# Kernel tuning notes

Measured on AMD Instinct MI355X. Metric: run time of the kernel, lower is better.

Reference implementation:

```python
import jax, jax.numpy as jnp
import numpy as np

MAX_ITER = 10
F_TOL = 1e-8
FREE_NUM = 100  # free_idx[1] + 1
OUT_DIM = 512


def setup_inputs() -> dict:
    key = jax.random.key(0)
    ks = jax.random.split(key, 13)
    f32 = jnp.float32
    b = jax.random.normal(ks[0], (64, 448), f32)
    # MLP params (nn.Linear convention: W [out, in], bias [out])
    W1 = jax.random.normal(ks[1], (1024, 448), f32) * 0.05
    b1 = jax.random.normal(ks[2], (1024,), f32) * 0.01
    W2 = jax.random.normal(ks[3], (1024, 1024), f32) * 0.03
    b2 = jax.random.normal(ks[4], (1024,), f32) * 0.01
    W3 = jax.random.normal(ks[5], (1024, 1024), f32) * 0.03
    b3 = jax.random.normal(ks[6], (1024,), f32) * 0.01
    W4 = jax.random.normal(ks[7], (512, 1024), f32) * 0.03
    b4 = jax.random.normal(ks[8], (512,), f32) * 0.01
    A = jax.random.normal(ks[9], (448, 512), f32) * 0.05
    WzProj = jax.random.normal(ks[10], (512, 512), f32) * 0.01  # contractive
    WbProj = jax.random.normal(ks[11], (512, 448), f32) * 0.05
    return {"b": b, "W1": W1, "b1": b1, "W2": W2, "b2": b2, "W3": W3,
            "b3": b3, "W4": W4, "b4": b4, "A": A, "WzProj": WzProj,
            "WbProj": WbProj}


def _projection(out, b0, A, WzProj, WbProj):
    # Fixed-point projection with on-device convergence flag + Jacobian accum
    bsz = out.shape[0]
    Bias = b0 @ WbProj.T                     # [bsz, d]
    col = jnp.arange(OUT_DIM)
    J0 = jnp.broadcast_to(jnp.eye(OUT_DIM, dtype=out.dtype),
                          (bsz, OUT_DIM, OUT_DIM))
    def cond(st):
        _, _, it, done = st
        return (it <= MAX_ITER) & (~done)
    def body(st):
        z, J, it, _ = st
        z = Bias + z @ WzProj.T
        # rows to clamp: negative AND in the ReLU (non-free) block
        mask = (z < 0) & (col >= FREE_NUM)                 # [bsz, d]
        J_iter = jnp.where(mask[:, :, None], 0.0, WzProj[None])  # [bsz,d,d]
        J = jnp.einsum('bij,bjk->bik', J_iter, J)          # bmm
        z = jnp.where(mask, 0.0, z)                        # u, relu(v)
        worst = jnp.max(jnp.abs(z @ A.T - b0))             # inf-norm residual
        return (z, J, it + 1, worst <= F_TOL)
    z, J, _, _ = jax.lax.while_loop(
        cond, body, (out, J0, jnp.int32(1), jnp.array(False)))
    return z, J


def reference(b, W1, b1, W2, b2, W3, b3, W4, b4, A, WzProj, WbProj):
    b0 = b
    h = b  # truncate_idx = [0, 448] -> full slice
    h = jax.nn.relu(h @ W1.T + b1)
    h = jax.nn.relu(h @ W2.T + b2)
    h = jax.nn.relu(h @ W3.T + b3)
    out = h @ W4.T + b4                                    # [bsz, 512]
    z_star, _ = _projection(out, b0, A, WzProj, WbProj)
    return (z_star, out)
```

## Files before the change

kernel.cpp:

```cpp
#include <hip/hip_runtime.h>


#define FREE0 100

__global__ __launch_bounds__(256) void transpose512(
    const float* __restrict__ Wz, float* __restrict__ WzT)
{
    __shared__ __align__(16) float Ts[64][65];
    const int t  = threadIdx.x;
    const int k0 = (blockIdx.x >> 3) * 64;
    const int n0 = (blockIdx.x & 7) * 64;
    #pragma unroll
    for (int i = 0; i < 4; ++i) {
        int f  = i * 256 + t;
        int r  = f >> 4;
        int c4 = (f & 15) << 2;
        const float4 v =
            *reinterpret_cast<const float4*>(Wz + (n0 + r) * 512 + k0 + c4);
        Ts[c4 + 0][r] = v.x; Ts[c4 + 1][r] = v.y;
        Ts[c4 + 2][r] = v.z; Ts[c4 + 3][r] = v.w;
    }
    __syncthreads();
    #pragma unroll
    for (int i = 0; i < 4; ++i) {
        int f   = i * 256 + t;
        int kk  = f >> 4;
        int nn4 = (f & 15) << 2;
        float4 w;
        w.x = Ts[kk][nn4 + 0]; w.y = Ts[kk][nn4 + 1];
        w.z = Ts[kk][nn4 + 2]; w.w = Ts[kk][nn4 + 3];
        *reinterpret_cast<float4*>(WzT + (k0 + kk) * 512 + n0 + nn4) = w;
    }
}

template <bool PRE>
__global__ __launch_bounds__(256) void linearSK(
    const float* __restrict__ X,
    const float* __restrict__ bp,
    const float* __restrict__ W,
    float* __restrict__ Cp,
    int N, int K, int chunk)
{
    __shared__ float Xs[64][65];
    __shared__ __align__(16) float Ws[64][16];

    const int t   = threadIdx.x;
    const int m   = t & 63;
    const int wv  = t >> 6;
    const int n0  = blockIdx.x * 16;
    const int kb  = blockIdx.y * chunk;
    const int ke  = (kb + chunk < K) ? (kb + chunk) : K;

    const int xc4 = (t & 15) << 2;
    const int xr0 = t >> 4;
    const int wnr = t >> 4;
    const int wkc = (t & 15) << 2;

    float4 xr[4];
    float4 wr;
    float4 bpv = {0.f, 0.f, 0.f, 0.f};

    auto issue = [&](int k0) {
        #pragma unroll
        for (int s = 0; s < 4; ++s)
            xr[s] = *reinterpret_cast<const float4*>(
                X + (s * 16 + xr0) * K + k0 + xc4);
        wr = *reinterpret_cast<const float4*>(W + (n0 + wnr) * K + k0 + wkc);
        if (PRE)
            bpv = *reinterpret_cast<const float4*>(bp + k0 + xc4);
    };

    issue(kb);
    float4 acc = {0.f, 0.f, 0.f, 0.f};

    for (int k0 = kb; k0 < ke; k0 += 64) {
        #pragma unroll
        for (int s = 0; s < 4; ++s) {
            float4 v = xr[s];
            if (PRE) {
                v.x = fmaxf(v.x + bpv.x, 0.f);
                v.y = fmaxf(v.y + bpv.y, 0.f);
                v.z = fmaxf(v.z + bpv.z, 0.f);
                v.w = fmaxf(v.w + bpv.w, 0.f);
            }
            const int row = s * 16 + xr0;
            Xs[xc4 + 0][row] = v.x; Xs[xc4 + 1][row] = v.y;
            Xs[xc4 + 2][row] = v.z; Xs[xc4 + 3][row] = v.w;
        }
        Ws[wkc + 0][wnr] = wr.x; Ws[wkc + 1][wnr] = wr.y;
        Ws[wkc + 2][wnr] = wr.z; Ws[wkc + 3][wnr] = wr.w;
        __syncthreads();

        if (k0 + 64 < ke) issue(k0 + 64);

        #pragma unroll 16
        for (int kk = 0; kk < 64; ++kk) {
            const float  xa = Xs[kk][m];
            const float4 w4 =
                *reinterpret_cast<const float4*>(&Ws[kk][wv * 4]);
            acc.x = fmaf(xa, w4.x, acc.x);
            acc.y = fmaf(xa, w4.y, acc.y);
            acc.z = fmaf(xa, w4.z, acc.z);
            acc.w = fmaf(xa, w4.w, acc.w);
        }
        __syncthreads();
    }

    float* cb = Cp + m * N + n0 + wv * 4;
    atomicAdd(cb + 0, acc.x);
    atomicAdd(cb + 1, acc.y);
    atomicAdd(cb + 2, acc.z);
    atomicAdd(cb + 3, acc.w);
}

__global__ __launch_bounds__(1024) void zloop2(
    const float* __restrict__ pre4,
    const float* __restrict__ b4,
    const float* __restrict__ WzT,
    const float* __restrict__ bz,
    float* __restrict__ dout)
{
    __shared__ float part[16][2][512];
    __shared__ float zs[512][2];
    __shared__ float bs[2][512];

    const int t   = threadIdx.x;
    const int bid = blockIdx.x;
    const int r   = t >> 9;
    const int c   = t & 511;
    const int row = bid * 2 + r;

    {
        const float z0 = pre4[row * 512 + c] + b4[c];
        dout[32768 + row * 512 + c] = z0;
        zs[c][r] = z0;
        bs[r][c] = bz[row * 512 + c];
    }
    __syncthreads();

    const int wv = t >> 6;
    const int l  = t & 63;
    const float* wbase = WzT + (wv * 32) * 512 + l * 8;

    for (int it = 0; it < 10; ++it) {
        float4 a00 = {0,0,0,0}, a01 = {0,0,0,0};
        float4 a10 = {0,0,0,0}, a11 = {0,0,0,0};
        const float* wp = wbase;
        #pragma unroll 4
        for (int kk = 0; kk < 32; ++kk) {
            const float4 w0 = *reinterpret_cast<const float4*>(wp);
            const float4 w1 = *reinterpret_cast<const float4*>(wp + 4);
            const float2 zr =
                *reinterpret_cast<const float2*>(&zs[wv * 32 + kk][0]);
            a00.x = fmaf(zr.x, w0.x, a00.x);
            a00.y = fmaf(zr.x, w0.y, a00.y);
            a00.z = fmaf(zr.x, w0.z, a00.z);
            a00.w = fmaf(zr.x, w0.w, a00.w);
            a01.x = fmaf(zr.x, w1.x, a01.x);
            a01.y = fmaf(zr.x, w1.y, a01.y);
            a01.z = fmaf(zr.x, w1.z, a01.z);
            a01.w = fmaf(zr.x, w1.w, a01.w);
            a10.x = fmaf(zr.y, w0.x, a10.x);
            a10.y = fmaf(zr.y, w0.y, a10.y);
            a10.z = fmaf(zr.y, w0.z, a10.z);
            a10.w = fmaf(zr.y, w0.w, a10.w);
            a11.x = fmaf(zr.y, w1.x, a11.x);
            a11.y = fmaf(zr.y, w1.y, a11.y);
            a11.z = fmaf(zr.y, w1.z, a11.z);
            a11.w = fmaf(zr.y, w1.w, a11.w);
            wp += 512;
        }
        *reinterpret_cast<float4*>(&part[wv][0][l * 8    ]) = a00;
        *reinterpret_cast<float4*>(&part[wv][0][l * 8 + 4]) = a01;
        *reinterpret_cast<float4*>(&part[wv][1][l * 8    ]) = a10;
        *reinterpret_cast<float4*>(&part[wv][1][l * 8 + 4]) = a11;
        __syncthreads();

        float v = bs[r][c];
        #pragma unroll
        for (int w = 0; w < 16; ++w) v += part[w][r][c];
        if (c >= FREE0) v = fmaxf(v, 0.f);
        zs[c][r] = v;
        if (it == 9) dout[row * 512 + c] = v;
        __syncthreads();
    }
}

extern "C" void kernel_launch(void* const* d_in, const int* in_sizes, int n_in,
                              void* d_out_v, int out_size, void* d_ws,
                              size_t ws_size, hipStream_t stream)
{
    const float* b  = (const float*)d_in[0];
    const float* W1 = (const float*)d_in[1];
    const float* b1 = (const float*)d_in[2];
    const float* W2 = (const float*)d_in[3];
    const float* b2 = (const float*)d_in[4];
    const float* W3 = (const float*)d_in[5];
    const float* b3 = (const float*)d_in[6];
    const float* W4 = (const float*)d_in[7];
    const float* b4 = (const float*)d_in[8];
    const float* Wz = (const float*)d_in[10];
    const float* Wb = (const float*)d_in[11];

    float* out = (float*)d_out_v;
    float* f   = (float*)d_ws;
    float* WzT  = f;
    float* z0b  = f + 262144;
    float* h1   = z0b;
    float* h2   = h1 + 65536;
    float* h3   = h2 + 65536;
    float* outp = h3 + 65536;
    float* bzv  = outp + 32768;

    hipMemsetAsync(z0b, 0, 262144 * sizeof(float), stream);
    transpose512<<<64, 256, 0, stream>>>(Wz, WzT);

    linearSK<false><<<dim3(64, 2), 256, 0, stream>>>(b,  nullptr, W1, h1,
                                                     1024, 448, 256);
    linearSK<true ><<<dim3(64, 4), 256, 0, stream>>>(h1, b1, W2, h2,
                                                     1024, 1024, 256);
    linearSK<true ><<<dim3(64, 4), 256, 0, stream>>>(h2, b2, W3, h3,
                                                     1024, 1024, 256);
    linearSK<true ><<<dim3(32, 4), 256, 0, stream>>>(h3, b3, W4, outp,
                                                     512, 1024, 256);
    linearSK<false><<<dim3(32, 2), 256, 0, stream>>>(b,  nullptr, Wb, bzv,
                                                     512, 448, 256);

    zloop2<<<32, 1024, 0, stream>>>(outp, b4, WzT, bzv, out);
}
```

Measured before the change: 247.1 us.

## Replace split-K atomic GEMMs with in-block K reduction and fused stage kernel

Replaces the split-K linear kernels, which relied on a memset and atomicAdd, with 1024-thread blocks that each compute 4 output columns across the full K. Partial sums are reduced in shared memory and the bias and ReLU are applied in the epilogue. The Wz transpose, the Wb projection and the first layer are merged into one stage0 launch, and the fixed-point loop now prefetches weights into registers. This removes the memset, the atomics and several launches, but the small-column-per-block layout reads W with strided scalar loads and reuses data less.

Result: slower. 477.7 us (+93.4%).

```diff
diff --git a/kernel.cpp b/kernel.cpp
--- a/kernel.cpp
+++ b/kernel.cpp
@@ -3,126 +3,118 @@
 
 #define FREE0 100
 
-__global__ __launch_bounds__(256) void transpose512(
-    const float* __restrict__ Wz, float* __restrict__ WzT)
-{
-    __shared__ __align__(16) float Ts[64][65];
+template <int K, bool RELU>
+__device__ __forceinline__ void layer_body(
+    const float* __restrict__ X, const float* __restrict__ W,
+    const float* __restrict__ bias, float* __restrict__ C,
+    int N, int n0, float* smem)
+{
+    constexpr int SL = K / 16;
+    float* Ws   = smem;
+    float* part = smem + K * 4;
+
     const int t  = threadIdx.x;
-    const int k0 = (blockIdx.x >> 3) * 64;
-    const int n0 = (blockIdx.x & 7) * 64;
+    const int wv = t >> 6;
+    const int l  = t & 63;
+
+    for (int base = t; base < 4 * K; base += 1024) {
+        const int k   = base >> 2;
+        const int col = base & 3;
+        Ws[base] = W[(n0 + col) * K + k];
+    }
+    float4 xr[SL / 4];
     #pragma unroll
-    for (int i = 0; i < 4; ++i) {
-        int f  = i * 256 + t;
-        int r  = f >> 4;
-        int c4 = (f & 15) << 2;
-        const float4 v =
-            *reinterpret_cast<const float4*>(Wz + (n0 + r) * 512 + k0 + c4);
-        Ts[c4 + 0][r] = v.x; Ts[c4 + 1][r] = v.y;
-        Ts[c4 + 2][r] = v.z; Ts[c4 + 3][r] = v.w;
-    }
+    for (int j = 0; j < SL / 4; ++j)
+        xr[j] = *reinterpret_cast<const float4*>(X + l * K + wv * SL + j * 4);
     __syncthreads();
+
+    float4 acc = {0.f, 0.f, 0.f, 0.f};
     #pragma unroll
-    for (int i = 0; i < 4; ++i) {
-        int f   = i * 256 + t;
-        int kk  = f >> 4;
-        int nn4 = (f & 15) << 2;
-        float4 w;
-        w.x = Ts[kk][nn4 + 0]; w.y = Ts[kk][nn4 + 1];
-        w.z = Ts[kk][nn4 + 2]; w.w = Ts[kk][nn4 + 3];
-        *reinterpret_cast<float4*>(WzT + (k0 + kk) * 512 + n0 + nn4) = w;
-    }
-}
-
-template <bool PRE>
-__global__ __launch_bounds__(256) void linearSK(
-    const float* __restrict__ X,
-    const float* __restrict__ bp,
-    const float* __restrict__ W,
-    float* __restrict__ Cp,
-    int N, int K, int chunk)
-{
-    __shared__ float Xs[64][65];
-    __shared__ __align__(16) float Ws[64][16];
-
+    for (int j = 0; j < SL / 4; ++j) {
+        #pragma unroll
+        for (int e = 0; e < 4; ++e) {
+            const int    k  = wv * SL + j * 4 + e;
+            const float4 w4 = *reinterpret_cast<const float4*>(&Ws[k * 4]);
+            const float  x  = (e == 0) ? xr[j].x : (e == 1) ? xr[j].y
+                            : (e == 2) ? xr[j].z : xr[j].w;
+            acc.x = fmaf(x, w4.x, acc.x);
+            acc.y = fmaf(x, w4.y, acc.y);
+            acc.z = fmaf(x, w4.z, acc.z);
+            acc.w = fmaf(x, w4.w, acc.w);
+        }
+    }
+    *reinterpret_cast<float4*>(&part[(wv * 64 + l) * 4]) = acc;
+    __syncthreads();
+
+    if (t < 256) {
+        const int row = t >> 2;
+        const int col = t & 3;
+        float s = 0.f;
+        #pragma unroll
+        for (int w = 0; w < 16; ++w)
+            s += part[w * 256 + t];
+        if (bias) s += bias[n0 + col];
+        if (RELU) s = fmaxf(s, 0.f);
+        C[row * N + n0 + col] = s;
+    }
+}
+
+__global__ __launch_bounds__(1024) void stage0(
+    const float* __restrict__ b,  const float* __restrict__ Wz,
+    const float* __restrict__ Wb, const float* __restrict__ W1,
+    const float* __restrict__ b1,
+    float* __restrict__ WzT, float* __restrict__ bzv, float* __restrict__ h1)
+{
+    __shared__ __align__(16) float smem[6144];
+    const int bid = blockIdx.x;
     const int t   = threadIdx.x;
-    const int m   = t & 63;
-    const int wv  = t >> 6;
-    const int n0  = blockIdx.x * 16;
-    const int kb  = blockIdx.y * chunk;
-    const int ke  = (kb + chunk < K) ? (kb + chunk) : K;
-
-    const int xc4 = (t & 15) << 2;
-    const int xr0 = t >> 4;
-    const int wnr = t >> 4;
-    const int wkc = (t & 15) << 2;
-
-    float4 xr[4];
-    float4 wr;
-    float4 bpv = {0.f, 0.f, 0.f, 0.f};
-
-    auto issue = [&](int k0) {
-        #pragma unroll
-        for (int s = 0; s < 4; ++s)
-            xr[s] = *reinterpret_cast<const float4*>(
-                X + (s * 16 + xr0) * K + k0 + xc4);
-        wr = *reinterpret_cast<const float4*>(W + (n0 + wnr) * K + k0 + wkc);
-        if (PRE)
-            bpv = *reinterpret_cast<const float4*>(bp + k0 + xc4);
-    };
-
-    issue(kb);
-    float4 acc = {0.f, 0.f, 0.f, 0.f};
-
-    for (int k0 = kb; k0 < ke; k0 += 64) {
-        #pragma unroll
-        for (int s = 0; s < 4; ++s) {
-            float4 v = xr[s];
-            if (PRE) {
-                v.x = fmaxf(v.x + bpv.x, 0.f);
-                v.y = fmaxf(v.y + bpv.y, 0.f);
-                v.z = fmaxf(v.z + bpv.z, 0.f);
-                v.w = fmaxf(v.w + bpv.w, 0.f);
-            }
-            const int row = s * 16 + xr0;
-            Xs[xc4 + 0][row] = v.x; Xs[xc4 + 1][row] = v.y;
-            Xs[xc4 + 2][row] = v.z; Xs[xc4 + 3][row] = v.w;
-        }
-        Ws[wkc + 0][wnr] = wr.x; Ws[wkc + 1][wnr] = wr.y;
-        Ws[wkc + 2][wnr] = wr.z; Ws[wkc + 3][wnr] = wr.w;
-        __syncthreads();
-
-        if (k0 + 64 < ke) issue(k0 + 64);
-
-        #pragma unroll 16
-        for (int kk = 0; kk < 64; ++kk) {
-            const float  xa = Xs[kk][m];
-            const float4 w4 =
-                *reinterpret_cast<const float4*>(&Ws[kk][wv * 4]);
-            acc.x = fmaf(xa, w4.x, acc.x);
-            acc.y = fmaf(xa, w4.y, acc.y);
-            acc.z = fmaf(xa, w4.z, acc.z);
-            acc.w = fmaf(xa, w4.w, acc.w);
-        }
-        __syncthreads();
-    }
-
-    float* cb = Cp + m * N + n0 + wv * 4;
-    atomicAdd(cb + 0, acc.x);
-    atomicAdd(cb + 1, acc.y);
-    atomicAdd(cb + 2, acc.z);
-    atomicAdd(cb + 3, acc.w);
-}
-
-__global__ __launch_bounds__(1024) void zloop2(
-    const float* __restrict__ pre4,
-    const float* __restrict__ b4,
+
+    if (bid < 16) {
+        const int r  = t >> 4;
+        const int c4 = (t & 15) << 2;
+        for (int tt = 0; tt < 4; ++tt) {
+            const int tile = bid * 4 + tt;
+            const int k0 = (tile >> 3) * 64;
+            const int n0 = (tile & 7) * 64;
+            const float4 v = *reinterpret_cast<const float4*>(
+                Wz + (n0 + r) * 512 + k0 + c4);
+            smem[(c4 + 0) * 65 + r] = v.x;
+            smem[(c4 + 1) * 65 + r] = v.y;
+            smem[(c4 + 2) * 65 + r] = v.z;
+            smem[(c4 + 3) * 65 + r] = v.w;
+            __syncthreads();
+            float4 w;
+            w.x = smem[r * 65 + c4 + 0];
+            w.y = smem[r * 65 + c4 + 1];
+            w.z = smem[r * 65 + c4 + 2];
+            w.w = smem[r * 65 + c4 + 3];
+            *reinterpret_cast<float4*>(WzT + (k0 + r) * 512 + n0 + c4) = w;
+            __syncthreads();
+        }
+    } else if (bid < 144) {
+        layer_body<448, false>(b, Wb, nullptr, bzv, 512, (bid - 16) * 4, smem);
+    } else {
+        layer_body<448, true>(b, W1, b1, h1, 1024, (bid - 144) * 4, smem);
+    }
+}
+
+template <int K, bool RELU>
+__global__ __launch_bounds__(1024) void layerK(
+    const float* __restrict__ X, const float* __restrict__ W,
+    const float* __restrict__ bias, float* __restrict__ C, int N)
+{
+    __shared__ __align__(16) float smem[K * 4 + 4096];
+    layer_body<K, RELU>(X, W, bias, C, N, blockIdx.x * 4, smem);
+}
+
+__global__ __launch_bounds__(1024) void zloop3(
+    const float* __restrict__ z0,
     const float* __restrict__ WzT,
     const float* __restrict__ bz,
     float* __restrict__ dout)
 {
-    __shared__ float part[16][2][512];
+    __shared__ float part[20][2][512];
     __shared__ float zs[512][2];
-    __shared__ float bs[2][512];
 
     const int t   = threadIdx.x;
     const int bid = blockIdx.x;
@@ -130,12 +122,8 @@
     const int c   = t & 511;
     const int row = bid * 2 + r;
 
-    {
-        const float z0 = pre4[row * 512 + c] + b4[c];
-        dout[32768 + row * 512 + c] = z0;
-        zs[c][r] = z0;
-        bs[r][c] = bz[row * 512 + c];
-    }
+    const float biasv = bz[row * 512 + c];
+    zs[c][r] = z0[row * 512 + c];
     __syncthreads();
 
     const int wv = t >> 6;
@@ -145,11 +133,24 @@
     for (int it = 0; it < 10; ++it) {
         float4 a00 = {0,0,0,0}, a01 = {0,0,0,0};
         float4 a10 = {0,0,0,0}, a11 = {0,0,0,0};
-        const float* wp = wbase;
-        #pragma unroll 4
+
+        float4 wa[4], wb[4];
+        #pragma unroll
+        for (int p = 0; p < 4; ++p) {
+            wa[p] = *reinterpret_cast<const float4*>(wbase + p * 512);
+            wb[p] = *reinterpret_cast<const float4*>(wbase + p * 512 + 4);
+        }
+        #pragma unroll
         for (int kk = 0; kk < 32; ++kk) {
-            const float4 w0 = *reinterpret_cast<const float4*>(wp);
-            const float4 w1 = *reinterpret_cast<const float4*>(wp + 4);
+            const int bsl = kk & 3;
+            const float4 w0 = wa[bsl];
+            const float4 w1 = wb[bsl];
+            if (kk < 28) {
+                wa[bsl] = *reinterpret_cast<const float4*>(
+                    wbase + (kk + 4) * 512);
+                wb[bsl] = *reinterpret_cast<const float4*>(
+                    wbase + (kk + 4) * 512 + 4);
+            }
             const float2 zr =
                 *reinterpret_cast<const float2*>(&zs[wv * 32 + kk][0]);
             a00.x = fmaf(zr.x, w0.x, a00.x);
@@ -168,7 +169,6 @@
             a11.y = fmaf(zr.y, w1.y, a11.y);
             a11.z = fmaf(zr.y, w1.z, a11.z);
             a11.w = fmaf(zr.y, w1.w, a11.w);
-            wp += 512;
         }
         *reinterpret_cast<float4*>(&part[wv][0][l * 8    ]) = a00;
         *reinterpret_cast<float4*>(&part[wv][0][l * 8 + 4]) = a01;
@@ -176,7 +176,7 @@
         *reinterpret_cast<float4*>(&part[wv][1][l * 8 + 4]) = a11;
         __syncthreads();
 
-        float v = bs[r][c];
+        float v = biasv;
         #pragma unroll
         for (int w = 0; w < 16; ++w) v += part[w][r][c];
         if (c >= FREE0) v = fmaxf(v, 0.f);
@@ -204,27 +204,16 @@
 
     float* out = (float*)d_out_v;
     float* f   = (float*)d_ws;
-    float* WzT  = f;
-    float* z0b  = f + 262144;
-    float* h1   = z0b;
-    float* h2   = h1 + 65536;
-    float* h3   = h2 + 65536;
-    float* outp = h3 + 65536;
-    float* bzv  = outp + 32768;
-
-    hipMemsetAsync(z0b, 0, 262144 * sizeof(float), stream);
-    transpose512<<<64, 256, 0, stream>>>(Wz, WzT);
-
-    linearSK<false><<<dim3(64, 2), 256, 0, stream>>>(b,  nullptr, W1, h1,
-                                                     1024, 448, 256);
-    linearSK<true ><<<dim3(64, 4), 256, 0, stream>>>(h1, b1, W2, h2,
-                                                     1024, 1024, 256);
-    linearSK<true ><<<dim3(64, 4), 256, 0, stream>>>(h2, b2, W3, h3,
-                                                     1024, 1024, 256);
-    linearSK<true ><<<dim3(32, 4), 256, 0, stream>>>(h3, b3, W4, outp,
-                                                     512, 1024, 256);
-    linearSK<false><<<dim3(32, 2), 256, 0, stream>>>(b,  nullptr, Wb, bzv,
-                                                     512, 448, 256);
-
-    zloop2<<<32, 1024, 0, stream>>>(outp, b4, WzT, bzv, out);
-}
+    float* WzT = f;  f += 512 * 512;
+    float* h1  = f;  f += 64 * 1024;
+    float* h2  = f;  f += 64 * 1024;
+    float* h3  = f;  f += 64 * 1024;
+    float* bzv = f;  f += 64 * 512;
+    float* outb = out + 32768;
+
+    stage0<<<400, 1024, 0, stream>>>(b, Wz, Wb, W1, b1, WzT, bzv, h1);
+    layerK<1024, true ><<<256, 1024, 0, stream>>>(h1, W2, b2, h2, 1024);
+    layerK<1024, true ><<<256, 1024, 0, stream>>>(h2, W3, b3, h3, 1024);
+    layerK<1024, false><<<128, 1024, 0, stream>>>(h3, W4, b4, outb, 512);
+    zloop3<<<32, 1024, 0, stream>>>(outb, WzT, bzv, out);
+}
```
